# Performance work log

Measured on AMD Instinct MI355X. Metric: run time of the kernel, lower is better.

The kernel has to match this reference:

```python
import jax, jax.numpy as jnp
import numpy as np

B, S = 32, 2048
DIM_ACTION = 32
DIM_STRUCT = 64
HIDDEN = 128  # mlp_hidden_dim default = dim_action * 4
EPS = 1e-12   # F.normalize eps


def l2norm(t):
    n = jnp.linalg.norm(t, axis=-1, keepdims=True)
    return t / jnp.maximum(n, EPS)


def setup_inputs() -> dict:
    key = jax.random.key(0)
    ks = jax.random.split(key, 9)
    sd = lambda fan_in: 1.0 / np.sqrt(fan_in)
    inp = {
        "actions": jax.random.normal(ks[0], (B, S, DIM_ACTION), dtype=jnp.float32),
        # MLP: dim_action -> hidden -> hidden -> dim_structure^2 (depth=2 hidden relu layers)
        "w0": jax.random.uniform(ks[1], (DIM_ACTION, HIDDEN), jnp.float32, -sd(DIM_ACTION), sd(DIM_ACTION)),
        "b0": jnp.zeros((HIDDEN,), jnp.float32),
        "w1": jax.random.uniform(ks[2], (HIDDEN, HIDDEN), jnp.float32, -sd(HIDDEN), sd(HIDDEN)),
        "b1": jnp.zeros((HIDDEN,), jnp.float32),
        "w2": jax.random.uniform(ks[3], (HIDDEN, DIM_STRUCT * DIM_STRUCT), jnp.float32, -sd(HIDDEN), sd(HIDDEN)),
        "b2": jnp.zeros((DIM_STRUCT * DIM_STRUCT,), jnp.float32),
        # RNN init hidden parameter [1, dim_structure], ~N(0, 0.01)
        "init_hidden": jax.random.normal(ks[4], (1, DIM_STRUCT), dtype=jnp.float32) * 0.01,
    }
    return inp


def reference(actions, w0, b0, w1, b1, w2, b2, init_hidden):
    # MLP to transitions: [B, S, d*d]
    h = jax.nn.relu(jnp.einsum("bsa,ah->bsh", actions, w0) + b0)
    h = jax.nn.relu(jnp.einsum("bsh,hk->bsk", h, w1) + b1)
    t = jnp.einsum("bsh,ho->bso", h, w2) + b2
    transitions = t.reshape(B, S, DIM_STRUCT, DIM_STRUCT)  # [B, S, i, j]

    # RNN: hidden_{t+1} = l2norm(relu(hidden_t @ T_t)), scanned over seq
    hidden0 = jnp.broadcast_to(l2norm(init_hidden), (B, DIM_STRUCT))

    def step(hidden, trans):  # trans: [B, i, j]
        hidden = jnp.einsum("bi,bij->bj", hidden, trans)
        hidden = l2norm(jax.nn.relu(hidden))
        return hidden, hidden

    trans_seq = jnp.swapaxes(transitions, 0, 1)  # [S, B, i, j]
    _, hiddens = jax.lax.scan(step, hidden0, trans_seq)  # [S, B, d]
    return jnp.swapaxes(hiddens, 0, 1)  # [B, S, d]
```

## Files before the change

kernel.cpp:

```cpp
#include <hip/hip_runtime.h>

#define B_ 32
#define S_ 2048
#define DA 32
#define DH 128
#define DS 64
#define DS2 4096
#define TKK 16

template <int CTRL>
__device__ __forceinline__ float dpp_add(float x) {
  int t = __builtin_amdgcn_update_dpp(0, __float_as_int(x), CTRL, 0xF, 0xF, true);
  return x + __int_as_float(t);
}
__device__ __forceinline__ float row_sum16(float x) {
  x = dpp_add<0xB1>(x);
  x = dpp_add<0x4E>(x);
  x = dpp_add<0x141>(x);
  x = dpp_add<0x140>(x);
  return x;
}

__device__ __forceinline__ void gl2lds16(const float* g, float* l) {
  __builtin_amdgcn_global_load_lds(
      (const __attribute__((address_space(1))) void*)g,
      (__attribute__((address_space(3))) void*)l, 16, 0, 0);
}

struct SharedRnn {
  float4 ring[6][16][64];
  int flags[6];
  int cons;
};
struct SharedGemm {
  float As[DH][128];
  float4 part[256][17];
};
struct SharedMlp {
  float a_t[DA][64];
  float w0_l[DA][DH];
  float h0t[DH][64];
};
union SharedU {
  SharedRnn r;
  SharedGemm g;
  SharedMlp m;
};

__device__ __forceinline__ void mlp_tile(
    const float* __restrict__ actions, const float* __restrict__ w0,
    const float* __restrict__ b0, const float* __restrict__ w1,
    const float* __restrict__ b1, float* __restrict__ h1t,
    int s_base, int M, int m0, SharedMlp& sm, int tid)
{
  {
    int tok = tid >> 3, kq = tid & 7;
    int tl = m0 + tok;
    int b = tl & 31, s = s_base + (tl >> 5);
    float4 v = *(const float4*)(actions + ((size_t)b * S_ + s) * DA + 4 * kq);
    sm.a_t[4 * kq + 0][tok] = v.x; sm.a_t[4 * kq + 1][tok] = v.y;
    sm.a_t[4 * kq + 2][tok] = v.z; sm.a_t[4 * kq + 3][tok] = v.w;
  }
#pragma unroll
  for (int q = 0; q < 2; ++q) {
    int g = tid + 512 * q;
    ((float4*)&sm.w0_l[0][0])[g] = ((const float4*)w0)[g];
  }
  __syncthreads();

  const int tm = tid & 15;
  const int tn = tid >> 4;

  float acc[4][4];
#pragma unroll
  for (int mi = 0; mi < 4; ++mi)
#pragma unroll
    for (int ni = 0; ni < 4; ++ni) acc[mi][ni] = 0.f;

#pragma unroll 4
  for (int k = 0; k < DA; ++k) {
    float4 a4 = *(const float4*)&sm.a_t[k][4 * tm];
    float4 w4 = *(const float4*)&sm.w0_l[k][4 * tn];
    float av[4] = {a4.x, a4.y, a4.z, a4.w};
    float wv[4] = {w4.x, w4.y, w4.z, w4.w};
#pragma unroll
    for (int mi = 0; mi < 4; ++mi)
#pragma unroll
      for (int ni = 0; ni < 4; ++ni) acc[mi][ni] += av[mi] * wv[ni];
  }
  {
    float4 b4 = *(const float4*)(b0 + 4 * tn);
    float bv[4] = {b4.x, b4.y, b4.z, b4.w};
#pragma unroll
    for (int mi = 0; mi < 4; ++mi)
#pragma unroll
      for (int ni = 0; ni < 4; ++ni)
        sm.h0t[4 * tn + ni][4 * tm + mi] = fmaxf(acc[mi][ni] + bv[ni], 0.f);
  }
  __syncthreads();

  float acc1[4][4];
#pragma unroll
  for (int mi = 0; mi < 4; ++mi)
#pragma unroll
    for (int ni = 0; ni < 4; ++ni) acc1[mi][ni] = 0.f;

#pragma unroll 4
  for (int k = 0; k < DH; ++k) {
    float4 h4 = *(const float4*)&sm.h0t[k][4 * tm];
    float4 w4 = *(const float4*)(w1 + (size_t)k * DH + 4 * tn);
    float av[4] = {h4.x, h4.y, h4.z, h4.w};
    float wv[4] = {w4.x, w4.y, w4.z, w4.w};
#pragma unroll
    for (int mi = 0; mi < 4; ++mi)
#pragma unroll
      for (int ni = 0; ni < 4; ++ni) acc1[mi][ni] += av[mi] * wv[ni];
  }
  {
    float4 b4 = *(const float4*)(b1 + 4 * tn);
    float bv[4] = {b4.x, b4.y, b4.z, b4.w};
#pragma unroll
    for (int ni = 0; ni < 4; ++ni) {
      float4 o;
      o.x = fmaxf(acc1[0][ni] + bv[ni], 0.f);
      o.y = fmaxf(acc1[1][ni] + bv[ni], 0.f);
      o.z = fmaxf(acc1[2][ni] + bv[ni], 0.f);
      o.w = fmaxf(acc1[3][ni] + bv[ni], 0.f);
      *(float4*)(h1t + (size_t)(4 * tn + ni) * M + m0 + 4 * tm) = o;
    }
  }
}

__device__ __forceinline__ void trans_loop(
    const float* __restrict__ h1t, const float* __restrict__ w2,
    const float* __restrict__ b2, float* __restrict__ trans,
    int M, int bi, SharedGemm& sg, int tid)
{
  const int w  = tid >> 6;
  const int lw = tid & 63;
  const int NJ = (M / 128) * (DS2 / 128);
  if (bi >= NJ) return;

  auto aloadF = [&](int j) {
    const int m0 = (j >> 5) * 128;
    const int rb = 16 * w;
    const int c4 = 4 * (lw & 31);
    const int ro = lw >> 5;
#pragma unroll
    for (int q = 0; q < 8; ++q) {
      const int kr = rb + 2 * q + ro;
      gl2lds16(h1t + (size_t)kr * M + m0 + c4, &sg.As[rb + 2 * q][0]);
    }
  };

  const int sub = tid & 255;
  const int khalf = tid >> 8;
  const int mg = sub >> 4;
  const int ng = sub & 15;
  const int kb = 64 * khalf;

  aloadF(bi);
  asm volatile("s_waitcnt vmcnt(0)" ::: "memory");
  __syncthreads();

  for (int j = bi; j < NJ; j += 224) {
    const int m0 = (j >> 5) * 128, n0 = (j & 31) * 128;

    float acc[8][8];
#pragma unroll
    for (int mi = 0; mi < 8; ++mi)
#pragma unroll
      for (int ni = 0; ni < 8; ++ni) acc[mi][ni] = 0.f;

    const float* w2p = w2 + (size_t)kb * DS2 + n0 + 4 * ng;
#pragma unroll 4
    for (int k8 = 0; k8 < 64; ++k8) {
      float4 b0v = *(const float4*)(w2p + (size_t)k8 * DS2);
      float4 b1v = *(const float4*)(w2p + (size_t)k8 * DS2 + 64);
      float4 a0 = *(const float4*)&sg.As[kb + k8][8 * mg];
      float4 a1 = *(const float4*)&sg.As[kb + k8][8 * mg + 4];
      float av[8] = {a0.x, a0.y, a0.z, a0.w, a1.x, a1.y, a1.z, a1.w};
      float bv[8] = {b0v.x, b0v.y, b0v.z, b0v.w, b1v.x, b1v.y, b1v.z, b1v.w};
#pragma unroll
      for (int mi = 0; mi < 8; ++mi)
#pragma unroll
        for (int ni = 0; ni < 8; ++ni) acc[mi][ni] += av[mi] * bv[ni];
    }
    __syncthreads();

    if (khalf) {
#pragma unroll
      for (int mi = 0; mi < 8; ++mi) {
        sg.part[sub][2 * mi] =
            make_float4(acc[mi][0], acc[mi][1], acc[mi][2], acc[mi][3]);
        sg.part[sub][2 * mi + 1] =
            make_float4(acc[mi][4], acc[mi][5], acc[mi][6], acc[mi][7]);
      }
    }
    if (j + 224 < NJ) aloadF(j + 224);
    __syncthreads();

    if (!khalf) {
      float4 bb0 = *(const float4*)(b2 + n0 + 4 * ng);
      float4 bb1 = *(const float4*)(b2 + n0 + 64 + 4 * ng);
      float bv[8] = {bb0.x, bb0.y, bb0.z, bb0.w, bb1.x, bb1.y, bb1.z, bb1.w};
#pragma unroll
      for (int mi = 0; mi < 8; ++mi) {
        float4 p0 = sg.part[sub][2 * mi];
        float4 p1 = sg.part[sub][2 * mi + 1];
        float pv[8] = {p0.x, p0.y, p0.z, p0.w, p1.x, p1.y, p1.z, p1.w};
        float* dst = trans + (size_t)(m0 + 8 * mg + mi) * DS2 + n0;
#pragma unroll
        for (int q = 0; q < 2; ++q) {
          float4 o;
          o.x = acc[mi][4 * q + 0] + pv[4 * q + 0] + bv[4 * q + 0];
          o.y = acc[mi][4 * q + 1] + pv[4 * q + 1] + bv[4 * q + 1];
          o.z = acc[mi][4 * q + 2] + pv[4 * q + 2] + bv[4 * q + 2];
          o.w = acc[mi][4 * q + 3] + pv[4 * q + 3] + bv[4 * q + 3];
          *(float4*)(dst + 64 * q + 4 * ng) = o;
        }
      }
    }
    asm volatile("s_waitcnt vmcnt(0)" ::: "memory");
    __syncthreads();
  }
}

__global__ __launch_bounds__(512) void k_mlp01(
    const float* __restrict__ actions, const float* __restrict__ w0,
    const float* __restrict__ b0, const float* __restrict__ w1,
    const float* __restrict__ b1, float* __restrict__ h1t,
    int s_base, int M)
{
  __shared__ SharedMlp sm;
  mlp_tile(actions, w0, b0, w1, b1, h1t, s_base, M, blockIdx.x * 64, sm,
           threadIdx.x);
}

__global__ __launch_bounds__(512, 1) void k_comb(
    const float* __restrict__ actions, const float* __restrict__ w0,
    const float* __restrict__ b0, const float* __restrict__ w1,
    const float* __restrict__ b1, const float* __restrict__ w2,
    const float* __restrict__ b2, const float* __restrict__ init_hidden,
    float* __restrict__ trans0, float* __restrict__ trans1,
    float* __restrict__ h1t0, float* __restrict__ h1t1,
    float* __restrict__ hstate, float* __restrict__ out,
    int c, int SC, int nch)
{
  __shared__ SharedU sh;
  const int tid = threadIdx.x;
  const int M = SC * 32;

  if (blockIdx.x >= 32) {
    const int bi = blockIdx.x - 32;
    if (c < nch) {
      const float* h1t = (c & 1) ? h1t1 : h1t0;
      float* trans = (c & 1) ? trans1 : trans0;
      trans_loop(h1t, w2, b2, trans, M, bi, sh.g, tid);
      if (c + 1 < nch) {
        __syncthreads();
        float* h1n = ((c + 1) & 1) ? h1t1 : h1t0;
        for (int j = bi; j < M / 64; j += 224) {
          mlp_tile(actions, w0, b0, w1, b1, h1n, (c + 1) * SC, M, j * 64,
                   sh.m, tid);
          __syncthreads();
        }
      }
    }
    return;
  }

  if (c == 0) return;
  const int cc = c - 1;
  const float* trans = (cc & 1) ? trans1 : trans0;
  const int s_base = cc * SC;
  const int wv = tid >> 6;
  const int lane = tid & 63;
  const int b = blockIdx.x;

  if (tid < 6) sh.r.flags[tid] = 0;
  if (tid == 6) sh.r.cons = 0;
  __syncthreads();

  const float* base = trans + (size_t)b * DS2;

  if (wv > 0) {
    if (wv <= 3) {
      const int p = wv - 1;
      int prev = -1;
      for (int s = p; s < SC; s += 3) {
        while (s - __hip_atomic_load(&sh.r.cons, __ATOMIC_RELAXED,
                                     __HIP_MEMORY_SCOPE_WORKGROUP) > 5)
          __builtin_amdgcn_s_sleep(2);
        const int slot = s % 6;
        const float* g = base + (size_t)s * (32 * DS2) + 4 * lane;
        float* l = (float*)&sh.r.ring[slot][0][0];
#pragma unroll
        for (int q = 0; q < 16; ++q)
          gl2lds16(g + q * 256, l + q * 256);
        if (prev >= 0) {
          asm volatile("s_waitcnt vmcnt(16)" ::: "memory");
          __hip_atomic_store(&sh.r.flags[prev % 6], prev + 1, __ATOMIC_RELAXED,
                             __HIP_MEMORY_SCOPE_WORKGROUP);
        }
        prev = s;
      }
      if (prev >= 0) {
        asm volatile("s_waitcnt vmcnt(0)" ::: "memory");
        __hip_atomic_store(&sh.r.flags[prev % 6], prev + 1, __ATOMIC_RELAXED,
                           __HIP_MEMORY_SCOPE_WORKGROUP);
      }
    }
  } else {
    const int d = lane >> 4;
    const int cq = lane & 15;
    const bool d1 = (d & 1), d2 = (d & 2);
    const int pb = lane & 48;

    float4 hq;
    if (cc == 0) {
      hq = *(const float4*)(init_hidden + 4 * cq);
      float ss0 = row_sum16(hq.x * hq.x + hq.y * hq.y + hq.z * hq.z + hq.w * hq.w);
      float iv0 = 1.0f / fmaxf(sqrtf(ss0), 1e-12f);
      hq.x *= iv0; hq.y *= iv0; hq.z *= iv0; hq.w *= iv0;
    } else {
      hq = *(const float4*)(hstate + b * DS + 4 * cq);
    }
    float inv_prev = 1.0f;

    float* outp = out + ((size_t)b * S_ + s_base) * DS + 4 * cq;
    int fpre = -1;
    for (int s = 0; s < SC; ++s) {
      const int slot = s % 6;
      if (fpre < s + 1) {
        while (__hip_atomic_load(&sh.r.flags[slot], __ATOMIC_ACQUIRE,
                                 __HIP_MEMORY_SCOPE_WORKGROUP) < s + 1)
          __builtin_amdgcn_s_sleep(0);
      }
      fpre = __hip_atomic_load(&sh.r.flags[(s + 1) % 6], __ATOMIC_ACQUIRE,
                               __HIP_MEMORY_SCOPE_WORKGROUP);

      float hsel = d2 ? (d1 ? hq.w : hq.z) : (d1 ? hq.y : hq.x);
      float ax = 0.f, ay = 0.f, az = 0.f, aw = 0.f;
#pragma unroll
      for (int q = 0; q < 16; ++q) {
        float4 t4 = sh.r.ring[slot][q][lane];
        float hb = __shfl(hsel, pb + q, 64);
        ax += hb * t4.x; ay += hb * t4.y;
        az += hb * t4.z; aw += hb * t4.w;
      }
      __hip_atomic_store(&sh.r.cons, s + 1, __ATOMIC_RELAXED,
                         __HIP_MEMORY_SCOPE_WORKGROUP);

      ax += __shfl_xor(ax, 16, 64); ax += __shfl_xor(ax, 32, 64);
      ay += __shfl_xor(ay, 16, 64); ay += __shfl_xor(ay, 32, 64);
      az += __shfl_xor(az, 16, 64); az += __shfl_xor(az, 32, 64);
      aw += __shfl_xor(aw, 16, 64); aw += __shfl_xor(aw, 32, 64);
      hq.x = fmaxf(ax * inv_prev, 0.f);
      hq.y = fmaxf(ay * inv_prev, 0.f);
      hq.z = fmaxf(az * inv_prev, 0.f);
      hq.w = fmaxf(aw * inv_prev, 0.f);
      float ss = row_sum16(hq.x * hq.x + hq.y * hq.y + hq.z * hq.z + hq.w * hq.w);
      float inv = 1.0f / fmaxf(sqrtf(ss), 1e-12f);
      if (d == 0) {
        float4 o;
        o.x = hq.x * inv; o.y = hq.y * inv; o.z = hq.z * inv; o.w = hq.w * inv;
        *(float4*)(outp + (size_t)s * DS) = o;
      }
      inv_prev = inv;
    }
    if (d == 0) {
      float4 o;
      o.x = hq.x * inv_prev; o.y = hq.y * inv_prev;
      o.z = hq.z * inv_prev; o.w = hq.w * inv_prev;
      *(float4*)(hstate + b * DS + 4 * cq) = o;
    }
  }
}

extern "C" void kernel_launch(void* const* d_in, const int* in_sizes, int n_in,
                              void* d_out, int out_size, void* d_ws, size_t ws_size,
                              hipStream_t stream) {
  const float* actions     = (const float*)d_in[0];
  const float* w0          = (const float*)d_in[1];
  const float* b0          = (const float*)d_in[2];
  const float* w1          = (const float*)d_in[3];
  const float* b1          = (const float*)d_in[4];
  const float* w2          = (const float*)d_in[5];
  const float* b2          = (const float*)d_in[6];
  const float* init_hidden = (const float*)d_in[7];
  float* out = (float*)d_out;

  int SC = 2048;
  while (SC > 4) {
    size_t need = 2 * ((size_t)SC * 32 * DS2 * 4 + (size_t)SC * 32 * DH * 4)
                + (size_t)B_ * DS * 4;
    if (need <= ws_size) break;
    SC >>= 1;
  }
  float* trans0 = (float*)d_ws;
  float* trans1 = trans0 + (size_t)SC * 32 * DS2;
  float* h1t0   = trans1 + (size_t)SC * 32 * DS2;
  float* h1t1   = h1t0 + (size_t)SC * 32 * DH;
  float* hstate = h1t1 + (size_t)SC * 32 * DH;

  const int M = SC * 32;
  const int nch = S_ / SC;

  hipLaunchKernelGGL(k_mlp01, dim3(M / 64), dim3(512), 0, stream,
                     actions, w0, b0, w1, b1, h1t0, 0, M);
  for (int c = 0; c <= nch; ++c) {
    hipLaunchKernelGGL(k_comb, dim3(256), dim3(512), 0, stream,
                       actions, w0, b0, w1, b1, w2, b2, init_hidden,
                       trans0, trans1, h1t0, h1t1, hstate, out, c, SC, nch);
  }
}
```

Baseline: 1.586 ms.

## Pin each GEMM block to one w2 column strip cached in LDS

```diff
diff --git a/kernel.cpp b/kernel.cpp
--- a/kernel.cpp
+++ b/kernel.cpp
@@ -6,7 +6,6 @@
 #define DH 128
 #define DS 64
 #define DS2 4096
-#define TKK 16
 
 template <int CTRL>
 __device__ __forceinline__ float dpp_add(float x) {
@@ -34,7 +33,8 @@
 };
 struct SharedGemm {
   float As[DH][128];
-  float4 part[256][17];
+  float Bs[DH][128];
+  float4 part[256][5];
 };
 struct SharedMlp {
   float a_t[DA][64];
@@ -134,15 +134,17 @@
 __device__ __forceinline__ void trans_loop(
     const float* __restrict__ h1t, const float* __restrict__ w2,
     const float* __restrict__ b2, float* __restrict__ trans,
-    int M, int bi, SharedGemm& sg, int tid)
+    int M, int x, SharedGemm& sg, int tid)
 {
   const int w  = tid >> 6;
   const int lw = tid & 63;
-  const int NJ = (M / 128) * (DS2 / 128);
-  if (bi >= NJ) return;
-
-  auto aloadF = [&](int j) {
-    const int m0 = (j >> 5) * 128;
+  const int strip = x / 7;
+  const int idx   = x % 7;
+  const int n0 = strip * 128;
+  const int MT = M / 128;
+
+  auto aloadF = [&](int mt) {
+    const int m0 = mt * 128;
     const int rb = 16 * w;
     const int c4 = 4 * (lw & 31);
     const int ro = lw >> 5;
@@ -152,6 +154,20 @@
       gl2lds16(h1t + (size_t)kr * M + m0 + c4, &sg.As[rb + 2 * q][0]);
     }
   };
+
+  {
+    const int rb = 16 * w;
+    const int c4 = 4 * (lw & 31);
+    const int ro = lw >> 5;
+#pragma unroll
+    for (int q = 0; q < 8; ++q) {
+      const int kr = rb + 2 * q + ro;
+      gl2lds16(w2 + (size_t)kr * DS2 + n0 + c4, &sg.Bs[rb + 2 * q][0]);
+    }
+  }
+  if (idx < MT) aloadF(idx);
+  asm volatile("s_waitcnt vmcnt(0)" ::: "memory");
+  __syncthreads();
 
   const int sub = tid & 255;
   const int khalf = tid >> 8;
@@ -159,12 +175,12 @@
   const int ng = sub & 15;
   const int kb = 64 * khalf;
 
-  aloadF(bi);
-  asm volatile("s_waitcnt vmcnt(0)" ::: "memory");
-  __syncthreads();
-
-  for (int j = bi; j < NJ; j += 224) {
-    const int m0 = (j >> 5) * 128, n0 = (j & 31) * 128;
+  float4 bb0 = *(const float4*)(b2 + n0 + 4 * ng);
+  float4 bb1 = *(const float4*)(b2 + n0 + 64 + 4 * ng);
+  float bvb[8] = {bb0.x, bb0.y, bb0.z, bb0.w, bb1.x, bb1.y, bb1.z, bb1.w};
+
+  for (int mt = idx; mt < MT; mt += 7) {
+    const int m0 = mt * 128;
 
     float acc[8][8];
 #pragma unroll
@@ -172,13 +188,15 @@
 #pragma unroll
       for (int ni = 0; ni < 8; ++ni) acc[mi][ni] = 0.f;
 
-    const float* w2p = w2 + (size_t)kb * DS2 + n0 + 4 * ng;
+    const float* asp = &sg.As[kb][0];
+    const float* bsp = &sg.Bs[kb][0];
+
 #pragma unroll 4
     for (int k8 = 0; k8 < 64; ++k8) {
-      float4 b0v = *(const float4*)(w2p + (size_t)k8 * DS2);
-      float4 b1v = *(const float4*)(w2p + (size_t)k8 * DS2 + 64);
-      float4 a0 = *(const float4*)&sg.As[kb + k8][8 * mg];
-      float4 a1 = *(const float4*)&sg.As[kb + k8][8 * mg + 4];
+      float4 a0 = *(const float4*)(asp + k8 * 128 + 8 * mg);
+      float4 a1 = *(const float4*)(asp + k8 * 128 + 8 * mg + 4);
+      float4 b0v = *(const float4*)(bsp + k8 * 128 + 4 * ng);
+      float4 b1v = *(const float4*)(bsp + k8 * 128 + 64 + 4 * ng);
       float av[8] = {a0.x, a0.y, a0.z, a0.w, a1.x, a1.y, a1.z, a1.w};
       float bv[8] = {b0v.x, b0v.y, b0v.z, b0v.w, b1v.x, b1v.y, b1v.z, b1v.w};
 #pragma unroll
@@ -188,38 +206,42 @@
     }
     __syncthreads();
 
-    if (khalf) {
-#pragma unroll
-      for (int mi = 0; mi < 8; ++mi) {
-        sg.part[sub][2 * mi] =
-            make_float4(acc[mi][0], acc[mi][1], acc[mi][2], acc[mi][3]);
-        sg.part[sub][2 * mi + 1] =
-            make_float4(acc[mi][4], acc[mi][5], acc[mi][6], acc[mi][7]);
-      }
-    }
-    if (j + 224 < NJ) aloadF(j + 224);
-    __syncthreads();
-
-    if (!khalf) {
-      float4 bb0 = *(const float4*)(b2 + n0 + 4 * ng);
-      float4 bb1 = *(const float4*)(b2 + n0 + 64 + 4 * ng);
-      float bv[8] = {bb0.x, bb0.y, bb0.z, bb0.w, bb1.x, bb1.y, bb1.z, bb1.w};
-#pragma unroll
-      for (int mi = 0; mi < 8; ++mi) {
-        float4 p0 = sg.part[sub][2 * mi];
-        float4 p1 = sg.part[sub][2 * mi + 1];
-        float pv[8] = {p0.x, p0.y, p0.z, p0.w, p1.x, p1.y, p1.z, p1.w};
-        float* dst = trans + (size_t)(m0 + 8 * mg + mi) * DS2 + n0;
-#pragma unroll
-        for (int q = 0; q < 2; ++q) {
-          float4 o;
-          o.x = acc[mi][4 * q + 0] + pv[4 * q + 0] + bv[4 * q + 0];
-          o.y = acc[mi][4 * q + 1] + pv[4 * q + 1] + bv[4 * q + 1];
-          o.z = acc[mi][4 * q + 2] + pv[4 * q + 2] + bv[4 * q + 2];
-          o.w = acc[mi][4 * q + 3] + pv[4 * q + 3] + bv[4 * q + 3];
-          *(float4*)(dst + 64 * q + 4 * ng) = o;
+    if (mt + 7 < MT) aloadF(mt + 7);
+
+#pragma unroll
+    for (int p = 0; p < 4; ++p) {
+      const int mi0 = 2 * p;
+      if (khalf) {
+        sg.part[sub][0] =
+            make_float4(acc[mi0][0], acc[mi0][1], acc[mi0][2], acc[mi0][3]);
+        sg.part[sub][1] =
+            make_float4(acc[mi0][4], acc[mi0][5], acc[mi0][6], acc[mi0][7]);
+        sg.part[sub][2] = make_float4(acc[mi0 + 1][0], acc[mi0 + 1][1],
+                                      acc[mi0 + 1][2], acc[mi0 + 1][3]);
+        sg.part[sub][3] = make_float4(acc[mi0 + 1][4], acc[mi0 + 1][5],
+                                      acc[mi0 + 1][6], acc[mi0 + 1][7]);
+      }
+      __syncthreads();
+      if (!khalf) {
+#pragma unroll
+        for (int r = 0; r < 2; ++r) {
+          const int mi = mi0 + r;
+          float4 p0 = sg.part[sub][2 * r];
+          float4 p1 = sg.part[sub][2 * r + 1];
+          float pv[8] = {p0.x, p0.y, p0.z, p0.w, p1.x, p1.y, p1.z, p1.w};
+          float* dst = trans + (size_t)(m0 + 8 * mg + mi) * DS2 + n0;
+#pragma unroll
+          for (int q = 0; q < 2; ++q) {
+            float4 o;
+            o.x = acc[mi][4 * q + 0] + pv[4 * q + 0] + bvb[4 * q + 0];
+            o.y = acc[mi][4 * q + 1] + pv[4 * q + 1] + bvb[4 * q + 1];
+            o.z = acc[mi][4 * q + 2] + pv[4 * q + 2] + bvb[4 * q + 2];
+            o.w = acc[mi][4 * q + 3] + pv[4 * q + 3] + bvb[4 * q + 3];
+            *(float4*)(dst + 64 * q + 4 * ng) = o;
+          }
         }
       }
+      __syncthreads();
     }
     asm volatile("s_waitcnt vmcnt(0)" ::: "memory");
     __syncthreads();
@@ -252,15 +274,15 @@
   const int M = SC * 32;
 
   if (blockIdx.x >= 32) {
-    const int bi = blockIdx.x - 32;
+    const int x = blockIdx.x - 32;
     if (c < nch) {
       const float* h1t = (c & 1) ? h1t1 : h1t0;
       float* trans = (c & 1) ? trans1 : trans0;
-      trans_loop(h1t, w2, b2, trans, M, bi, sh.g, tid);
+      trans_loop(h1t, w2, b2, trans, M, x, sh.g, tid);
       if (c + 1 < nch) {
         __syncthreads();
         float* h1n = ((c + 1) & 1) ? h1t1 : h1t0;
-        for (int j = bi; j < M / 64; j += 224) {
+        for (int j = x; j < M / 64; j += 224) {
           mlp_tile(actions, w0, b0, w1, b1, h1n, (c + 1) * SC, M, j * 64,
                    sh.m, tid);
           __syncthreads();
```

New measurement: 1.604 ms. No clear change (+1.1%).
